# Performance work log

Measured on AMD Instinct MI355X. Metric: run time of the kernel, lower is better.

The kernel has to match this reference:

```python
import jax, jax.numpy as jnp
import numpy as np

N_NODES = 100000
N_DIH = 1000000
SCALAR_DIM = 128
HIDDEN = 64
ATTR_DIM = 3


def setup_inputs() -> dict:
    key = jax.random.key(0)
    ks = jax.random.split(key, 10)
    x = jax.random.normal(ks[0], (N_NODES, SCALAR_DIM), dtype=jnp.float32)
    quadra_index = jax.random.randint(ks[1], (4, N_DIH), 0, N_NODES, dtype=jnp.int32)
    quadra_attr = jax.random.normal(ks[2], (N_DIH, ATTR_DIM), dtype=jnp.float32)
    d_in = SCALAR_DIM * 2 + ATTR_DIM
    W1 = jax.random.normal(ks[3], (d_in, HIDDEN), dtype=jnp.float32) / np.sqrt(d_in)
    b1 = jnp.zeros((HIDDEN,), dtype=jnp.float32)
    W2 = jax.random.normal(ks[4], (HIDDEN, HIDDEN), dtype=jnp.float32) / np.sqrt(HIDDEN)
    b2 = jnp.zeros((HIDDEN,), dtype=jnp.float32)
    W3 = jax.random.normal(ks[5], (HIDDEN, SCALAR_DIM), dtype=jnp.float32) / np.sqrt(HIDDEN)
    b3 = jnp.zeros((SCALAR_DIM,), dtype=jnp.float32)
    # o3.Linear on pure scalars ('128x0e'->'128x0e') is a bias-free linear map
    Wout = jax.random.normal(ks[6], (SCALAR_DIM, SCALAR_DIM), dtype=jnp.float32) / np.sqrt(SCALAR_DIM)
    return {"x": x, "quadra_index": quadra_index, "quadra_attr": quadra_attr,
            "W1": W1, "b1": b1, "W2": W2, "b2": b2, "W3": W3, "b3": b3, "Wout": Wout}


def _scatter_mean(msgs, idx, num_segments):
    sums = jax.ops.segment_sum(msgs, idx, num_segments=num_segments)
    counts = jax.ops.segment_sum(jnp.ones((msgs.shape[0],), msgs.dtype), idx,
                                 num_segments=num_segments)
    return sums / jnp.maximum(counts, 1.0)[:, None]


def reference(x, quadra_index, quadra_attr, W1, b1, W2, b2, W3, b3, Wout):
    n = x.shape[0]
    x_scalar = x[:, :SCALAR_DIM]
    i, j, k, l = quadra_index[0], quadra_index[1], quadra_index[2], quadra_index[3]
    # gather endpoints, concat with dihedral attrs: [E, 2*D + 3]
    dih_in = jnp.concatenate([x_scalar[i], x_scalar[l], quadra_attr], axis=-1)
    h = jax.nn.silu(dih_in @ W1 + b1)
    h = jax.nn.silu(h @ W2 + b2)
    msgs = h @ W3 + b3  # [E, D]
    aggr_j = _scatter_mean(msgs, j, n)
    aggr_k = _scatter_mean(msgs, k, n)
    aggr = (aggr_j + aggr_k) * 0.5
    return aggr @ Wout
```

## Files before the change

kernel.cpp:

```cpp
#include <hip/hip_runtime.h>

#define N_NODES    100000
#define N_DIH      1000000
#define SCALAR_DIM 128
#define HIDDEN     64
#define ATTR_DIM   3

typedef short v8s __attribute__((ext_vector_type(8)));
typedef float v4f __attribute__((ext_vector_type(4)));
typedef _Float16 v8h __attribute__((ext_vector_type(8)));

__device__ __forceinline__ float silu(float v) {
    return __fdividef(v, 1.0f + __expf(-v));
}

__device__ __forceinline__ unsigned short bf16_rne(float f) {
    unsigned int u = __float_as_uint(f);
    u = (u + 0x7FFFu + ((u >> 16) & 1u)) >> 16;
    return (unsigned short)u;
}

__device__ __forceinline__ float2 bf2_to_f2(unsigned int v) {
    float2 r;
    r.x = __uint_as_float(v << 16);
    r.y = __uint_as_float(v & 0xffff0000u);
    return r;
}

#define PREP_W   112
#define PREP_W34 33
#define PREP_G   64
#define PREP_H   3907
#define PREP_XB  12500
#define PREP_MAIN (PREP_W + PREP_W34 + PREP_G + PREP_H)
#define PREP_ALL  (PREP_MAIN + PREP_XB)

__global__ void prep_kernel(const float* __restrict__ x, unsigned short* __restrict__ xb,
                            const float* __restrict__ W1, const float* __restrict__ W2,
                            const float* __restrict__ W3, const float* __restrict__ b1,
                            const float* __restrict__ b3,
                            const float* __restrict__ Wout,
                            unsigned short* __restrict__ W1f, unsigned short* __restrict__ W2f,
                            unsigned short* __restrict__ W3f, unsigned short* __restrict__ W1g,
                            float* __restrict__ W34, float* __restrict__ b34,
                            float* __restrict__ PK,
                            const int* __restrict__ qidx,
                            int* __restrict__ cnt_j, int* __restrict__ cnt_k,
                            int* __restrict__ rank_j, int* __restrict__ rank_k) {
    const int b = blockIdx.x;
    if (b < PREP_W) {
        const int tid = b * 256 + threadIdx.x;
        if (tid < 16384) {
            const int j = tid & 7, lane = (tid >> 3) & 63, t = tid >> 9;
            const int k = (t >> 2) * 32 + ((lane >> 4) << 3) + j;
            const int n = (t & 3) * 16 + (lane & 15);
            W1f[tid] = bf16_rne(W1[k * 64 + n]);
        } else if (tid < 20480) {
            const int i = tid - 16384;
            const int j = i & 7, lane = (i >> 3) & 63, t = i >> 9;
            const int k = (t >> 2) * 32 + ((lane >> 4) << 3) + j;
            const int n = (t & 3) * 16 + (lane & 15);
            W2f[i] = bf16_rne(W2[k * 64 + n]);
        } else if (tid < 28672) {
            const int i = tid - 20480;
            const int j = i & 7, lane = (i >> 3) & 63, t = i >> 9;
            const int k = (t >> 3) * 32 + ((lane >> 4) << 3) + j;
            const int n = (t & 7) * 16 + (lane & 15);
            W3f[i] = bf16_rne(W3[k * 128 + n]);
        }
    } else if (b < PREP_W + PREP_W34) {
        const int t34 = (b - PREP_W) * 256 + threadIdx.x;
        if (t34 < 8192) {
            const int r = t34 >> 7, c = t34 & 127;
            float s = 0.f;
            #pragma unroll 4
            for (int m = 0; m < 128; ++m) s += W3[r * 128 + m] * Wout[m * 128 + c];
            W34[t34] = s;
        } else if (t34 < 8320) {
            const int c = t34 - 8192;
            float s = 0.f;
            #pragma unroll 4
            for (int m = 0; m < 128; ++m) s += b3[m] * Wout[m * 128 + c];
            b34[c] = s;
        } else if (t34 < 8384) {
            const int c = t34 - 8320;
            PK[c * 4 + 0] = W1[256 * 64 + c];
            PK[c * 4 + 1] = W1[257 * 64 + c];
            PK[c * 4 + 2] = W1[258 * 64 + c];
            PK[c * 4 + 3] = b1[c];
        }
    } else if (b < PREP_W + PREP_W34 + PREP_G) {
        const int i = (b - PREP_W - PREP_W34) * 256 + threadIdx.x;
        const int j = i & 7, lane = (i >> 3) & 63, t = i >> 9;
        const int k = (t >> 3) * 32 + ((lane >> 4) << 3) + j;
        const int n = (t & 7) * 16 + (lane & 15);
        const float w = (n < 64) ? W1[k * 64 + n] : W1[(128 + k) * 64 + (n - 64)];
        W1g[i] = bf16_rne(w);
    } else if (b < PREP_MAIN) {
        const int t = (b - PREP_W - PREP_W34 - PREP_G) * 256 + threadIdx.x;
        if (t < N_DIH) {
            const int rj = atomicAdd(&cnt_j[qidx[N_DIH + t]], 1);
            const int rk = atomicAdd(&cnt_k[qidx[2 * N_DIH + t]], 1);
            if (rank_j != nullptr) {
                rank_j[t] = rj;
                rank_k[t] = rk;
            }
        }
    } else {
        const int t = (b - PREP_MAIN) * 256 + threadIdx.x;
        const float4 v = *(const float4*)&x[(size_t)t * 4];
        ushort4 o;
        o.x = bf16_rne(v.x); o.y = bf16_rne(v.y); o.z = bf16_rne(v.z); o.w = bf16_rne(v.w);
        *(ushort4*)&xb[(size_t)t * 4] = o;
    }
}

__global__ __launch_bounds__(1024) void scan_kernel(const int* __restrict__ cnt_j,
                                                    const int* __restrict__ cnt_k,
                                                    int* __restrict__ off_j, int* __restrict__ off_k) {
    const int* cnt = blockIdx.x ? cnt_k : cnt_j;
    int* off = blockIdx.x ? off_k : off_j;
    __shared__ int wtot[17];
    const int tid = threadIdx.x, lane = tid & 63, wv = tid >> 6;
    int carry = 0;
    for (int base = 0; base < N_NODES; base += 1024) {
        const int i = base + tid;
        const int v = (i < N_NODES) ? cnt[i] : 0;
        int inc = v;
        #pragma unroll
        for (int o = 1; o < 64; o <<= 1) {
            const int t = __shfl_up(inc, o);
            if (lane >= o) inc += t;
        }
        if (lane == 63) wtot[wv] = inc;
        __syncthreads();
        if (tid == 0) {
            int run = 0;
            #pragma unroll
            for (int w = 0; w < 16; ++w) { const int t = wtot[w]; wtot[w] = run; run += t; }
            wtot[16] = run;
        }
        __syncthreads();
        const int excl = inc - v + wtot[wv] + carry;
        if (i < N_NODES) off[i] = excl;
        carry += wtot[16];
        __syncthreads();
    }
    if (tid == 0) off[N_NODES] = carry;
}

__global__ void permute_kernel(const int* __restrict__ qidx,
                               const int* __restrict__ off_j, const int* __restrict__ off_k,
                               const int* __restrict__ rank_j, const int* __restrict__ rank_k,
                               int* __restrict__ perm_j, int* __restrict__ perm_k) {
    const int t = blockIdx.x * blockDim.x + threadIdx.x;
    if (t < N_DIH) {
        const int j = qidx[N_DIH + t];
        perm_j[off_j[j] + rank_j[t]] = t;
        const int k = qidx[2 * N_DIH + t];
        perm_k[off_k[k] + rank_k[t]] = t;
    }
}

#define UVW 3125

__global__ __launch_bounds__(256, 4) void uv_kernel(
    const float* __restrict__ x, const unsigned short* __restrict__ W1g,
    _Float16* __restrict__ uv)
{
    const int tid = threadIdx.x, lane = tid & 63, wv = tid >> 6;
    const int g = blockIdx.x * 4 + wv;
    if (g >= UVW) return;
    const int D0 = g * 32;
    const int m16 = lane & 15, quad = lane >> 4;
    const int r0 = D0 + m16, r1 = D0 + 16 + m16;

    v4f acc[2][8];
    #pragma unroll
    for (int mt = 0; mt < 2; ++mt)
        #pragma unroll
        for (int nt = 0; nt < 8; ++nt) acc[mt][nt] = (v4f){0.f, 0.f, 0.f, 0.f};

    #pragma unroll
    for (int kc = 0; kc < 4; ++kc) {
        const int co = kc * 32 + quad * 8;
        v8s a0, a1;
        {
            const float4 f0 = *(const float4*)&x[(size_t)r0 * 128 + co];
            const float4 f1 = *(const float4*)&x[(size_t)r0 * 128 + co + 4];
            a0[0] = (short)bf16_rne(f0.x); a0[1] = (short)bf16_rne(f0.y);
            a0[2] = (short)bf16_rne(f0.z); a0[3] = (short)bf16_rne(f0.w);
            a0[4] = (short)bf16_rne(f1.x); a0[5] = (short)bf16_rne(f1.y);
            a0[6] = (short)bf16_rne(f1.z); a0[7] = (short)bf16_rne(f1.w);
        }
        {
            const float4 f0 = *(const float4*)&x[(size_t)r1 * 128 + co];
            const float4 f1 = *(const float4*)&x[(size_t)r1 * 128 + co + 4];
            a1[0] = (short)bf16_rne(f0.x); a1[1] = (short)bf16_rne(f0.y);
            a1[2] = (short)bf16_rne(f0.z); a1[3] = (short)bf16_rne(f0.w);
            a1[4] = (short)bf16_rne(f1.x); a1[5] = (short)bf16_rne(f1.y);
            a1[6] = (short)bf16_rne(f1.z); a1[7] = (short)bf16_rne(f1.w);
        }
        #pragma unroll
        for (int nt = 0; nt < 8; ++nt) {
            const v8s bf = *(const v8s*)(W1g + ((kc * 8 + nt) * 64 + lane) * 8);
            acc[0][nt] = __builtin_amdgcn_mfma_f32_16x16x32_bf16(a0, bf, acc[0][nt], 0, 0, 0);
            acc[1][nt] = __builtin_amdgcn_mfma_f32_16x16x32_bf16(a1, bf, acc[1][nt], 0, 0, 0);
        }
    }
    #pragma unroll
    for (int mt = 0; mt < 2; ++mt)
        #pragma unroll
        for (int nt = 0; nt < 8; ++nt) {
            const int c = nt * 16 + m16;
            #pragma unroll
            for (int reg = 0; reg < 4; ++reg) {
                const int n = D0 + mt * 16 + quad * 4 + reg;
                uv[(size_t)n * 128 + c] = (_Float16)acc[mt][nt][reg];
            }
        }
}

#define NW16 62500

__global__ __launch_bounds__(256, 6) void mlp2s_kernel(
    const _Float16* __restrict__ uv, const int* __restrict__ qidx,
    const float* __restrict__ attr, const float* __restrict__ PK,
    const unsigned short* __restrict__ W2f, const float* __restrict__ b2,
    const int* __restrict__ off_j, const int* __restrict__ off_k,
    const int* __restrict__ rank_j, const int* __restrict__ rank_k,
    unsigned short* __restrict__ h2j, unsigned short* __restrict__ h2k)
{
    __shared__ __align__(16) unsigned short hbuf[4][1024];
    const int tid = threadIdx.x, lane = tid & 63, wv = tid >> 6;
    const int g = blockIdx.x * 4 + wv;
    const int D0 = g * 16;
    const int m16 = lane & 15, quad = lane >> 4;
    unsigned short* hs = hbuf[wv];

    const int d = D0 + m16;
    const int irow = qidx[d];
    const int lrow = qidx[3 * N_DIH + d];
    const int jn = qidx[N_DIH + d];
    const int kn = qidx[2 * N_DIH + d];
    const int pj = off_j[jn] + rank_j[d];
    const int pk = off_k[kn] + rank_k[d];

    const _Float16* up = uv + (size_t)irow * 128 + quad * 8;
    const _Float16* vp = uv + (size_t)lrow * 128 + 64 + quad * 8;
    const v8h u0 = *(const v8h*)(up + 0);
    const v8h u1 = *(const v8h*)(up + 32);
    const v8h w0 = *(const v8h*)(vp + 0);
    const v8h w1 = *(const v8h*)(vp + 32);
    const float a0 = attr[(size_t)d * 3 + 0];
    const float a1 = attr[(size_t)d * 3 + 1];
    const float a2 = attr[(size_t)d * 3 + 2];

    const int cb = quad * 8;
    v8s af0, af1;
    #pragma unroll
    for (int e = 0; e < 8; ++e) {
        const float4 pk0 = *(const float4*)&PK[(size_t)(cb + e) * 4];
        const float s0 = (float)u0[e] + (float)w0[e] + pk0.x * a0 + pk0.y * a1 + pk0.z * a2 + pk0.w;
        af0[e] = (short)bf16_rne(silu(s0));
        const float4 pk1 = *(const float4*)&PK[(size_t)(32 + cb + e) * 4];
        const float s1 = (float)u1[e] + (float)w1[e] + pk1.x * a0 + pk1.y * a1 + pk1.z * a2 + pk1.w;
        af1[e] = (short)bf16_rne(silu(s1));
    }

    v4f acc2[4];
    #pragma unroll
    for (int nt = 0; nt < 4; ++nt) acc2[nt] = (v4f){0.f, 0.f, 0.f, 0.f};
    #pragma unroll
    for (int nt = 0; nt < 4; ++nt) {
        const v8s bA = *(const v8s*)(W2f + ((nt) * 64 + lane) * 8);
        const v8s bB = *(const v8s*)(W2f + ((4 + nt) * 64 + lane) * 8);
        acc2[nt] = __builtin_amdgcn_mfma_f32_16x16x32_bf16(af0, bA, acc2[nt], 0, 0, 0);
        acc2[nt] = __builtin_amdgcn_mfma_f32_16x16x32_bf16(af1, bB, acc2[nt], 0, 0, 0);
    }

    #pragma unroll
    for (int nt = 0; nt < 4; ++nt) {
        const int c = nt * 16 + m16;
        const float b2c = b2[c];
        #pragma unroll
        for (int reg = 0; reg < 4; ++reg) {
            const int row = quad * 4 + reg;
            hs[row * 64 + c] = bf16_rne(silu(acc2[nt][reg] + b2c));
        }
    }
    const int sub = lane & 7;
    #pragma unroll
    for (int i = 0; i < 2; ++i) {
        const int row = i * 8 + (lane >> 3);
        const int pjr = __shfl(pj, row);
        const int pkr = __shfl(pk, row);
        const v8s rowv = *(const v8s*)(hs + i * 512 + lane * 8);
        *(v8s*)(h2j + (size_t)pjr * 64 + sub * 8) = rowv;
        *(v8s*)(h2k + (size_t)pkr * 64 + sub * 8) = rowv;
    }
}

__global__ __launch_bounds__(256, 8) void mlp2_kernel(
    const _Float16* __restrict__ uv, const int* __restrict__ qidx,
    const float* __restrict__ attr, const float* __restrict__ PK,
    const unsigned short* __restrict__ W2f, const float* __restrict__ b2,
    unsigned short* __restrict__ h2)
{
    __shared__ __align__(16) unsigned short hbuf[4][1024];
    const int tid = threadIdx.x, lane = tid & 63, wv = tid >> 6;
    const int g = blockIdx.x * 4 + wv;
    const int D0 = g * 16;
    const int m16 = lane & 15, quad = lane >> 4;
    unsigned short* hs = hbuf[wv];

    const int d = D0 + m16;
    const int irow = qidx[d];
    const int lrow = qidx[3 * N_DIH + d];

    const _Float16* up = uv + (size_t)irow * 128 + quad * 8;
    const _Float16* vp = uv + (size_t)lrow * 128 + 64 + quad * 8;
    const v8h u0 = *(const v8h*)(up + 0);
    const v8h u1 = *(const v8h*)(up + 32);
    const v8h w0 = *(const v8h*)(vp + 0);
    const v8h w1 = *(const v8h*)(vp + 32);
    const float a0 = attr[(size_t)d * 3 + 0];
    const float a1 = attr[(size_t)d * 3 + 1];
    const float a2 = attr[(size_t)d * 3 + 2];

    const int cb = quad * 8;
    v8s af0, af1;
    #pragma unroll
    for (int e = 0; e < 8; ++e) {
        const float4 pk0 = *(const float4*)&PK[(size_t)(cb + e) * 4];
        const float s0 = (float)u0[e] + (float)w0[e] + pk0.x * a0 + pk0.y * a1 + pk0.z * a2 + pk0.w;
        af0[e] = (short)bf16_rne(silu(s0));
        const float4 pk1 = *(const float4*)&PK[(size_t)(32 + cb + e) * 4];
        const float s1 = (float)u1[e] + (float)w1[e] + pk1.x * a0 + pk1.y * a1 + pk1.z * a2 + pk1.w;
        af1[e] = (short)bf16_rne(silu(s1));
    }

    v4f acc2[4];
    #pragma unroll
    for (int nt = 0; nt < 4; ++nt) acc2[nt] = (v4f){0.f, 0.f, 0.f, 0.f};
    #pragma unroll
    for (int nt = 0; nt < 4; ++nt) {
        const v8s bA = *(const v8s*)(W2f + ((nt) * 64 + lane) * 8);
        const v8s bB = *(const v8s*)(W2f + ((4 + nt) * 64 + lane) * 8);
        acc2[nt] = __builtin_amdgcn_mfma_f32_16x16x32_bf16(af0, bA, acc2[nt], 0, 0, 0);
        acc2[nt] = __builtin_amdgcn_mfma_f32_16x16x32_bf16(af1, bB, acc2[nt], 0, 0, 0);
    }

    #pragma unroll
    for (int nt = 0; nt < 4; ++nt) {
        const int c = nt * 16 + m16;
        const float b2c = b2[c];
        #pragma unroll
        for (int reg = 0; reg < 4; ++reg) {
            const int row = quad * 4 + reg;
            hs[row * 64 + c] = bf16_rne(silu(acc2[nt][reg] + b2c));
        }
    }
    #pragma unroll
    for (int i = 0; i < 2; ++i) {
        const v8s row16 = *(const v8s*)(hs + i * 512 + lane * 8);
        *(v8s*)(h2 + (size_t)D0 * 64 + i * 512 + lane * 8) = row16;
    }
}

#define NWAVES 31250

__global__ __launch_bounds__(256, 8) void mlp12_kernel(
    const unsigned short* __restrict__ xb, const int* __restrict__ qidx,
    const float* __restrict__ attr,
    const float* __restrict__ W1, const float* __restrict__ b1,
    const float* __restrict__ b2,
    const unsigned short* __restrict__ W1f, const unsigned short* __restrict__ W2f,
    unsigned short* __restrict__ h2)
{
    __shared__ __align__(16) unsigned short hbuf[4][1024];
    const int tid  = threadIdx.x;
    const int lane = tid & 63;
    const int wv   = tid >> 6;
    const int g    = blockIdx.x * 4 + wv;
    const int D0   = g * 16;
    const int m16  = lane & 15;
    const int quad = lane >> 4;
    unsigned short* hs = hbuf[wv];

    const int irow = qidx[D0 + m16];
    const int lrow = qidx[3 * N_DIH + D0 + m16];

    v4f acc[4];
    #pragma unroll
    for (int nt = 0; nt < 4; ++nt) acc[nt] = (v4f){0.f, 0.f, 0.f, 0.f};

    #pragma unroll
    for (int kc = 0; kc < 8; ++kc) {
        const int side = kc >> 2;
        const int coff = (kc & 3) * 32 + quad * 8;
        const int r0 = side ? lrow : irow;
        const v8s a0 = *(const v8s*)(xb + (size_t)r0 * 128 + coff);
        #pragma unroll
        for (int nt = 0; nt < 4; ++nt) {
            const v8s b = *(const v8s*)(W1f + ((kc * 4 + nt) * 64 + lane) * 8);
            acc[nt] = __builtin_amdgcn_mfma_f32_16x16x32_bf16(a0, b, acc[nt], 0, 0, 0);
        }
    }

    #pragma unroll
    for (int nt = 0; nt < 4; ++nt) {
        const int c = nt * 16 + m16;
        const float b1c = b1[c];
        const float wa0 = W1[256 * 64 + c];
        const float wa1 = W1[257 * 64 + c];
        const float wa2 = W1[258 * 64 + c];
        const int quadp = (nt * 2 + (m16 >> 3)) & 3;
        const int jp    = m16 & 7;
        const int kc2   = nt >> 1;
        #pragma unroll
        for (int reg = 0; reg < 4; ++reg) {
            const int r = quad * 4 + reg;
            const int d = D0 + r;
            float v = acc[nt][reg] + b1c
                    + attr[(size_t)d * 3 + 0] * wa0
                    + attr[(size_t)d * 3 + 1] * wa1
                    + attr[(size_t)d * 3 + 2] * wa2;
            v = silu(v);
            hs[kc2 * 512 + (r + 16 * quadp) * 8 + jp] = bf16_rne(v);
        }
    }

    v4f acc2[4];
    #pragma unroll
    for (int nt = 0; nt < 4; ++nt) acc2[nt] = (v4f){0.f, 0.f, 0.f, 0.f};

    #pragma unroll
    for (int kc = 0; kc < 2; ++kc) {
        const v8s a0 = *(const v8s*)(hs + kc * 512 + lane * 8);
        #pragma unroll
        for (int nt = 0; nt < 4; ++nt) {
            const v8s b = *(const v8s*)(W2f + ((kc * 4 + nt) * 64 + lane) * 8);
            acc2[nt] = __builtin_amdgcn_mfma_f32_16x16x32_bf16(a0, b, acc2[nt], 0, 0, 0);
        }
    }

    #pragma unroll
    for (int nt = 0; nt < 4; ++nt) {
        const int c = nt * 16 + m16;
        const float b2c = b2[c];
        #pragma unroll
        for (int reg = 0; reg < 4; ++reg) {
            const int row = quad * 4 + reg;
            hs[row * 64 + c] = bf16_rne(silu(acc2[nt][reg] + b2c));
        }
    }
    #pragma unroll
    for (int i = 0; i < 2; ++i) {
        const v8s row16 = *(const v8s*)(hs + i * 512 + lane * 8);
        *(v8s*)(h2 + (size_t)D0 * 64 + i * 512 + lane * 8) = row16;
    }
}

__global__ __launch_bounds__(256, 2) void aggregate_seq(
    const unsigned short* __restrict__ h2j, const unsigned short* __restrict__ h2k,
    const int* __restrict__ off_j, const int* __restrict__ off_k,
    const float* __restrict__ W34, const float* __restrict__ b34,
    float* __restrict__ out)
{
    __shared__ float a_lds[64 * 132];
    const int tid    = threadIdx.x;
    const int lane   = tid & 63;
    const int wv     = __builtin_amdgcn_readfirstlane(tid >> 6);
    const int base   = blockIdx.x * 64;
    const int half   = lane >> 5;
    const int lane31 = lane & 31;

    for (int p = 0; p < 16; ++p) {
        const int ln = wv * 16 + p;
        const int n  = base + ln;
        float sx = 0.f, sy = 0.f, bf = 0.f;
        if (n < N_NODES) {
            int cj, ck;
            {
                const int e0 = off_j[n], e1 = off_j[n + 1];
                cj = e1 - e0;
                float ax = 0.f, ay = 0.f;
                int e = e0;
                for (; e + 4 <= e1; e += 4) {
                    const float2 fA = bf2_to_f2(*(const unsigned int*)(h2j + (size_t)(e + half) * 64 + lane31 * 2));
                    const float2 fB = bf2_to_f2(*(const unsigned int*)(h2j + (size_t)(e + 2 + half) * 64 + lane31 * 2));
                    ax += fA.x + fB.x; ay += fA.y + fB.y;
                }
                if (e + 2 <= e1) {
                    const float2 f = bf2_to_f2(*(const unsigned int*)(h2j + (size_t)(e + half) * 64 + lane31 * 2));
                    ax += f.x; ay += f.y;
                    e += 2;
                }
                if (e < e1 && half == 0) {
                    const float2 f = bf2_to_f2(*(const unsigned int*)(h2j + (size_t)e * 64 + lane31 * 2));
                    ax += f.x; ay += f.y;
                }
                ax += __shfl_xor(ax, 32);
                ay += __shfl_xor(ay, 32);
                const float inv = 1.0f / (float)max(cj, 1);
                sx += ax * inv; sy += ay * inv;
            }
            {
                const int e0 = off_k[n], e1 = off_k[n + 1];
                ck = e1 - e0;
                float ax = 0.f, ay = 0.f;
                int e = e0;
                for (; e + 4 <= e1; e += 4) {
                    const float2 fA = bf2_to_f2(*(const unsigned int*)(h2k + (size_t)(e + half) * 64 + lane31 * 2));
                    const float2 fB = bf2_to_f2(*(const unsigned int*)(h2k + (size_t)(e + 2 + half) * 64 + lane31 * 2));
                    ax += fA.x + fB.x; ay += fA.y + fB.y;
                }
                if (e + 2 <= e1) {
                    const float2 f = bf2_to_f2(*(const unsigned int*)(h2k + (size_t)(e + half) * 64 + lane31 * 2));
                    ax += f.x; ay += f.y;
                    e += 2;
                }
                if (e < e1 && half == 0) {
                    const float2 f = bf2_to_f2(*(const unsigned int*)(h2k + (size_t)e * 64 + lane31 * 2));
                    ax += f.x; ay += f.y;
                }
                ax += __shfl_xor(ax, 32);
                ay += __shfl_xor(ay, 32);
                const float inv = 1.0f / (float)max(ck, 1);
                sx += ax * inv; sy += ay * inv;
            }
            bf = 0.5f * ((float)(cj > 0) + (float)(ck > 0));
        }
        if (half == 0) {
            float2 w; w.x = sx * 0.5f; w.y = sy * 0.5f;
            *(float2*)&a_lds[ln * 132 + 2 * lane31] = w;
            if (lane31 == 0) a_lds[ln * 132 + 128] = bf;
        }
    }
    __syncthreads();

    const int co = wv * 32;
    const float bfv = a_lds[lane * 132 + 128];
    float acc[32];
    #pragma unroll
    for (int c = 0; c < 32; ++c) acc[c] = bfv * b34[co + c];
    const float* ap = &a_lds[lane * 132];
    #pragma unroll 2
    for (int d = 0; d < 64; d += 4) {
        const float4 av = *(const float4*)&ap[d];
        const float* w0 = &W34[(d + 0) * 128 + co];
        const float* w1 = w0 + 128;
        const float* w2 = w0 + 256;
        const float* w3 = w0 + 384;
        #pragma unroll
        for (int c = 0; c < 32; ++c)
            acc[c] += av.x * w0[c] + av.y * w1[c] + av.z * w2[c] + av.w * w3[c];
    }
    __syncthreads();
    #pragma unroll
    for (int c = 0; c < 32; c += 4)
        *(float4*)&a_lds[lane * 132 + co + c] = make_float4(acc[c], acc[c+1], acc[c+2], acc[c+3]);
    __syncthreads();
    const int q4 = lane31 << 2;
    #pragma unroll
    for (int p = 0; p < 8; ++p) {
        const int ln = wv * 16 + p * 2 + half;
        const int n  = base + ln;
        if (n < N_NODES)
            *(float4*)&out[(size_t)n * 128 + q4] = *(const float4*)&a_lds[ln * 132 + q4];
    }
}

__global__ __launch_bounds__(256, 4) void aggregate_out64(
    const unsigned short* __restrict__ h2,
    const int* __restrict__ off_j, const int* __restrict__ off_k,
    const int* __restrict__ perm_j, const int* __restrict__ perm_k,
    const float* __restrict__ W34, const float* __restrict__ b34,
    float* __restrict__ out)
{
    __shared__ float a_lds[64 * 132];
    const int tid    = threadIdx.x;
    const int lane   = tid & 63;
    const int wv     = __builtin_amdgcn_readfirstlane(tid >> 6);
    const int base   = blockIdx.x * 64;
    const int half   = lane >> 5;
    const int lane31 = lane & 31;

#define AGG_BATCH(B, permp, e, e1, ax, ay) \
    if (e + B <= e1) { \
        int dd[B]; \
        _Pragma("unroll") \
        for (int q = 0; q < B; ++q) dd[q] = permp[e + q]; \
        unsigned int rr[B]; \
        _Pragma("unroll") \
        for (int q = 0; q < B; ++q) \
            rr[q] = *(const unsigned int*)(h2 + (size_t)dd[q] * 64 + lane31 * 2); \
        _Pragma("unroll") \
        for (int q = 0; q < B; ++q) { \
            const float2 f = bf2_to_f2(rr[q]); \
            ax += f.x; ay += f.y; \
        } \
        e += B; \
    }

    for (int p = 0; p < 8; ++p) {
        const int ln = wv * 16 + p * 2 + half;
        const int n  = base + ln;
        float sx = 0.f, sy = 0.f, bf = 0.f;
        if (n < N_NODES) {
            const int ej0 = off_j[n], ej1 = off_j[n + 1];
            const int ek0 = off_k[n], ek1 = off_k[n + 1];
            const int cj = ej1 - ej0, ck = ek1 - ek0;
            float axj = 0.f, ayj = 0.f, axk = 0.f, ayk = 0.f;
            int ej = ej0, ek = ek0;
            while (ej + 8 <= ej1 && ek + 8 <= ek1) {
                int dj[8], dk[8];
                #pragma unroll
                for (int q = 0; q < 8; ++q) { dj[q] = perm_j[ej + q]; dk[q] = perm_k[ek + q]; }
                unsigned int rj[8], rk[8];
                #pragma unroll
                for (int q = 0; q < 8; ++q) {
                    rj[q] = *(const unsigned int*)(h2 + (size_t)dj[q] * 64 + lane31 * 2);
                    rk[q] = *(const unsigned int*)(h2 + (size_t)dk[q] * 64 + lane31 * 2);
                }
                #pragma unroll
                for (int q = 0; q < 8; ++q) {
                    const float2 fj = bf2_to_f2(rj[q]); axj += fj.x; ayj += fj.y;
                    const float2 fk = bf2_to_f2(rk[q]); axk += fk.x; ayk += fk.y;
                }
                ej += 8; ek += 8;
            }
            for (; ej + 8 <= ej1; ) { AGG_BATCH(8, perm_j, ej, ej1, axj, ayj) }
            AGG_BATCH(4, perm_j, ej, ej1, axj, ayj)
            AGG_BATCH(2, perm_j, ej, ej1, axj, ayj)
            AGG_BATCH(1, perm_j, ej, ej1, axj, ayj)
            for (; ek + 8 <= ek1; ) { AGG_BATCH(8, perm_k, ek, ek1, axk, ayk) }
            AGG_BATCH(4, perm_k, ek, ek1, axk, ayk)
            AGG_BATCH(2, perm_k, ek, ek1, axk, ayk)
            AGG_BATCH(1, perm_k, ek, ek1, axk, ayk)
            const float invj = 1.0f / (float)max(cj, 1);
            const float invk = 1.0f / (float)max(ck, 1);
            sx = axj * invj + axk * invk;
            sy = ayj * invj + ayk * invk;
            bf = 0.5f * ((float)(cj > 0) + (float)(ck > 0));
        }
        float2 w; w.x = sx * 0.5f; w.y = sy * 0.5f;
        *(float2*)&a_lds[ln * 132 + 2 * lane31] = w;
        if (lane31 == 0) a_lds[ln * 132 + 128] = bf;
    }
#undef AGG_BATCH
    __syncthreads();

    const int co = wv * 32;
    const float bfv = a_lds[lane * 132 + 128];
    float acc[32];
    #pragma unroll
    for (int c = 0; c < 32; ++c) acc[c] = bfv * b34[co + c];
    const float* ap = &a_lds[lane * 132];
    #pragma unroll 2
    for (int d = 0; d < 64; d += 4) {
        const float4 av = *(const float4*)&ap[d];
        const float* w0 = &W34[(d + 0) * 128 + co];
        const float* w1 = w0 + 128;
        const float* w2 = w0 + 256;
        const float* w3 = w0 + 384;
        #pragma unroll
        for (int c = 0; c < 32; ++c)
            acc[c] += av.x * w0[c] + av.y * w1[c] + av.z * w2[c] + av.w * w3[c];
    }
    __syncthreads();
    #pragma unroll
    for (int c = 0; c < 32; c += 4)
        *(float4*)&a_lds[lane * 132 + co + c] = make_float4(acc[c], acc[c+1], acc[c+2], acc[c+3]);
    __syncthreads();
    const int q4 = lane31 << 2;
    #pragma unroll
    for (int p = 0; p < 8; ++p) {
        const int ln = wv * 16 + p * 2 + half;
        const int n  = base + ln;
        if (n < N_NODES)
            *(float4*)&out[(size_t)n * 128 + q4] = *(const float4*)&a_lds[ln * 132 + q4];
    }
}

__global__ void scale_kernel(const int* __restrict__ cnt_j, const int* __restrict__ cnt_k,
                             float* __restrict__ scale_j, float* __restrict__ scale_k) {
    int n = blockIdx.x * blockDim.x + threadIdx.x;
    if (n < N_NODES) {
        scale_j[n] = 0.5f / (float)max(cnt_j[n], 1);
        scale_k[n] = 0.5f / (float)max(cnt_k[n], 1);
    }
}

__global__ __launch_bounds__(256, 3) void mlp_mfma_atomic(
    const unsigned short* __restrict__ xb, const int* __restrict__ qidx,
    const float* __restrict__ attr,
    const float* __restrict__ W1, const float* __restrict__ b1,
    const float* __restrict__ b2, const float* __restrict__ b3,
    const unsigned short* __restrict__ W1f, const unsigned short* __restrict__ W2f,
    const unsigned short* __restrict__ W3f,
    const float* __restrict__ scale_j, const float* __restrict__ scale_k,
    float* __restrict__ aggr)
{
    __shared__ __align__(16) unsigned short hbuf[4][4096];
    const int tid  = threadIdx.x;
    const int lane = tid & 63;
    const int wv   = tid >> 6;
    const int g    = blockIdx.x * 4 + wv;
    if (g >= NWAVES) return;
    const int D0   = g * 32;
    const int m16  = lane & 15;
    const int quad = lane >> 4;
    unsigned short* hs = hbuf[wv];

    int irow[2], lrow[2];
    irow[0] = qidx[D0 + m16];
    irow[1] = qidx[D0 + 16 + m16];
    lrow[0] = qidx[3 * N_DIH + D0 + m16];
    lrow[1] = qidx[3 * N_DIH + D0 + 16 + m16];

    v4f acc[2][4];
    #pragma unroll
    for (int mt = 0; mt < 2; ++mt)
        #pragma unroll
        for (int nt = 0; nt < 4; ++nt) acc[mt][nt] = (v4f){0.f, 0.f, 0.f, 0.f};
    #pragma unroll
    for (int kc = 0; kc < 8; ++kc) {
        const int side = kc >> 2;
        const int coff = (kc & 3) * 32 + quad * 8;
        const int r0 = side ? lrow[0] : irow[0];
        const int r1 = side ? lrow[1] : irow[1];
        const v8s a0 = *(const v8s*)(xb + (size_t)r0 * 128 + coff);
        const v8s a1 = *(const v8s*)(xb + (size_t)r1 * 128 + coff);
        #pragma unroll
        for (int nt = 0; nt < 4; ++nt) {
            const v8s b = *(const v8s*)(W1f + ((kc * 4 + nt) * 64 + lane) * 8);
            acc[0][nt] = __builtin_amdgcn_mfma_f32_16x16x32_bf16(a0, b, acc[0][nt], 0, 0, 0);
            acc[1][nt] = __builtin_amdgcn_mfma_f32_16x16x32_bf16(a1, b, acc[1][nt], 0, 0, 0);
        }
    }
    #pragma unroll
    for (int mt = 0; mt < 2; ++mt) {
        #pragma unroll
        for (int nt = 0; nt < 4; ++nt) {
            const int c = nt * 16 + m16;
            const float b1c = b1[c];
            const float wa0 = W1[256 * 64 + c];
            const float wa1 = W1[257 * 64 + c];
            const float wa2 = W1[258 * 64 + c];
            const int quadp = (nt * 2 + (m16 >> 3)) & 3;
            const int jp    = m16 & 7;
            const int kc2   = nt >> 1;
            #pragma unroll
            for (int reg = 0; reg < 4; ++reg) {
                const int r = quad * 4 + reg;
                const int d = D0 + mt * 16 + r;
                float v = acc[mt][nt][reg] + b1c
                        + attr[(size_t)d * 3 + 0] * wa0
                        + attr[(size_t)d * 3 + 1] * wa1
                        + attr[(size_t)d * 3 + 2] * wa2;
                v = silu(v);
                hs[mt * 1024 + kc2 * 512 + (r + 16 * quadp) * 8 + jp] = bf16_rne(v);
            }
        }
    }
    v4f acc2[2][4];
    #pragma unroll
    for (int mt = 0; mt < 2; ++mt)
        #pragma unroll
        for (int nt = 0; nt < 4; ++nt) acc2[mt][nt] = (v4f){0.f, 0.f, 0.f, 0.f};
    #pragma unroll
    for (int kc = 0; kc < 2; ++kc) {
        const v8s a0 = *(const v8s*)(hs +        kc * 512 + lane * 8);
        const v8s a1 = *(const v8s*)(hs + 1024 + kc * 512 + lane * 8);
        #pragma unroll
        for (int nt = 0; nt < 4; ++nt) {
            const v8s b = *(const v8s*)(W2f + ((kc * 4 + nt) * 64 + lane) * 8);
            acc2[0][nt] = __builtin_amdgcn_mfma_f32_16x16x32_bf16(a0, b, acc2[0][nt], 0, 0, 0);
            acc2[1][nt] = __builtin_amdgcn_mfma_f32_16x16x32_bf16(a1, b, acc2[1][nt], 0, 0, 0);
        }
    }
    #pragma unroll
    for (int mt = 0; mt < 2; ++mt) {
        #pragma unroll
        for (int nt = 0; nt < 4; ++nt) {
            const float b2c = b2[nt * 16 + m16];
            const int quadp = (nt * 2 + (m16 >> 3)) & 3;
            const int jp    = m16 & 7;
            const int kc2   = nt >> 1;
            #pragma unroll
            for (int reg = 0; reg < 4; ++reg) {
                const int r = quad * 4 + reg;
                const float v = silu(acc2[mt][nt][reg] + b2c);
                hs[2048 + mt * 1024 + kc2 * 512 + (r + 16 * quadp) * 8 + jp] = bf16_rne(v);
            }
        }
    }
    v4f acc3[2][8];
    #pragma unroll
    for (int mt = 0; mt < 2; ++mt)
        #pragma unroll
        for (int nt = 0; nt < 8; ++nt) acc3[mt][nt] = (v4f){0.f, 0.f, 0.f, 0.f};
    #pragma unroll
    for (int kc = 0; kc < 2; ++kc) {
        const v8s a0 = *(const v8s*)(hs + 2048 +        kc * 512 + lane * 8);
        const v8s a1 = *(const v8s*)(hs + 2048 + 1024 + kc * 512 + lane * 8);
        #pragma unroll
        for (int nt = 0; nt < 8; ++nt) {
            const v8s b = *(const v8s*)(W3f + ((kc * 8 + nt) * 64 + lane) * 8);
            acc3[0][nt] = __builtin_amdgcn_mfma_f32_16x16x32_bf16(a0, b, acc3[0][nt], 0, 0, 0);
            acc3[1][nt] = __builtin_amdgcn_mfma_f32_16x16x32_bf16(a1, b, acc3[1][nt], 0, 0, 0);
        }
    }
    #pragma unroll
    for (int mt = 0; mt < 2; ++mt) {
        int jn[4], kn[4]; float sjv[4], skv[4];
        #pragma unroll
        for (int reg = 0; reg < 4; ++reg) {
            const int d = D0 + mt * 16 + quad * 4 + reg;
            jn[reg] = qidx[N_DIH + d];
            kn[reg] = qidx[2 * N_DIH + d];
            sjv[reg] = scale_j[jn[reg]];
            skv[reg] = scale_k[kn[reg]];
        }
        #pragma unroll
        for (int nt = 0; nt < 8; ++nt) {
            const int c = nt * 16 + m16;
            const float b3c = b3[c];
            #pragma unroll
            for (int reg = 0; reg < 4; ++reg) {
                const float v = acc3[mt][nt][reg] + b3c;
                atomicAdd(&aggr[(size_t)jn[reg] * 128 + c], v * sjv[reg]);
                atomicAdd(&aggr[(size_t)kn[reg] * 128 + c], v * skv[reg]);
            }
        }
    }
}

#define OB    256
#define OTILE 64
__global__ __launch_bounds__(OB, 2) void out_kernel(const float* __restrict__ aggr,
                                                    const float* __restrict__ Wout,
                                                    float* __restrict__ out) {
    __shared__ float a_lds[OTILE * 132];
    const int tid  = threadIdx.x;
    const int lane = tid & 63;
    const int wv   = __builtin_amdgcn_readfirstlane(tid >> 6);
    const int base = blockIdx.x * OTILE;
    const int half = lane >> 5;
    const int q4   = (lane & 31) << 2;
    #pragma unroll
    for (int p = 0; p < 8; ++p) {
        const int ln = wv * 16 + p * 2 + half;
        const int n  = base + ln;
        float4 v = make_float4(0.f, 0.f, 0.f, 0.f);
        if (n < N_NODES) v = *(const float4*)&aggr[(size_t)n * 128 + q4];
        *(float4*)&a_lds[ln * 132 + q4] = v;
    }
    __syncthreads();
    const int c0 = wv * 32;
    float acc[32];
    #pragma unroll
    for (int c = 0; c < 32; ++c) acc[c] = 0.0f;
    const float* ap = &a_lds[lane * 132];
    #pragma unroll 2
    for (int d = 0; d < 128; d += 4) {
        const float4 av = *(const float4*)&ap[d];
        const float* w0 = &Wout[(d + 0) * 128 + c0];
        const float* w1 = &Wout[(d + 1) * 128 + c0];
        const float* w2 = &Wout[(d + 2) * 128 + c0];
        const float* w3 = &Wout[(d + 3) * 128 + c0];
        #pragma unroll
        for (int c = 0; c < 32; ++c)
            acc[c] += av.x * w0[c] + av.y * w1[c] + av.z * w2[c] + av.w * w3[c];
    }
    __syncthreads();
    #pragma unroll
    for (int c = 0; c < 32; c += 4)
        *(float4*)&a_lds[lane * 132 + c0 + c] = make_float4(acc[c], acc[c+1], acc[c+2], acc[c+3]);
    __syncthreads();
    #pragma unroll
    for (int p = 0; p < 8; ++p) {
        const int ln = wv * 16 + p * 2 + half;
        const int n  = base + ln;
        if (n < N_NODES)
            *(float4*)&out[(size_t)n * 128 + q4] = *(const float4*)&a_lds[ln * 132 + q4];
    }
}

extern "C" void kernel_launch(void* const* d_in, const int* in_sizes, int n_in,
                              void* d_out, int out_size, void* d_ws, size_t ws_size,
                              hipStream_t stream) {
    const float* x    = (const float*)d_in[0];
    const int*   qidx = (const int*)d_in[1];
    const float* attr = (const float*)d_in[2];
    const float* W1   = (const float*)d_in[3];
    const float* b1   = (const float*)d_in[4];
    const float* W2   = (const float*)d_in[5];
    const float* b2   = (const float*)d_in[6];
    const float* W3   = (const float*)d_in[7];
    const float* b3   = (const float*)d_in[8];
    const float* Wout = (const float*)d_in[9];
    float* out = (float*)d_out;
    float* wsf = (float*)d_ws;

    const size_t words = ws_size / 4;
    if (words >= (size_t)79300000) {
        size_t o = 0;
        unsigned short* h2j = (unsigned short*)wsf;          o += 32000000;
        unsigned short* h2k = (unsigned short*)(wsf + o);    o += 32000000;
        _Float16* uvp = (_Float16*)(wsf + o);                o += 12800000;
        unsigned short* W1f = (unsigned short*)(wsf + o);    o += 8192;
        unsigned short* W2f = (unsigned short*)(wsf + o);    o += 2048;
        unsigned short* W3f = (unsigned short*)(wsf + o);    o += 4096;
        unsigned short* W1g = (unsigned short*)(wsf + o);    o += 8192;
        float* W34  = wsf + o;                               o += 8192;
        float* b34  = wsf + o;                               o += 128;
        float* PK   = wsf + o;                               o += 256;
        int* cnt_j  = (int*)(wsf + o);                       o += 100000;
        int* cnt_k  = (int*)(wsf + o);                       o += 100000;
        int* off_j  = (int*)(wsf + o);                       o += 100001;
        int* off_k  = (int*)(wsf + o);                       o += 100001;
        int* rank_j = (int*)(wsf + o);                       o += 1000000;
        int* rank_k = (int*)(wsf + o);                       o += 1000000;

        hipMemsetAsync(cnt_j, 0, (size_t)200000 * sizeof(int), stream);
        prep_kernel<<<PREP_MAIN, 256, 0, stream>>>(
            x, h2j , W1, W2, W3, b1, b3, Wout,
            W1f, W2f, W3f, W1g, W34, b34, PK, qidx, cnt_j, cnt_k, rank_j, rank_k);
        scan_kernel<<<2, 1024, 0, stream>>>(cnt_j, cnt_k, off_j, off_k);
        uv_kernel<<<(UVW + 3) / 4, 256, 0, stream>>>(x, W1g, uvp);
        mlp2s_kernel<<<NW16 / 4, 256, 0, stream>>>(
            uvp, qidx, attr, PK, W2f, b2, off_j, off_k, rank_j, rank_k, h2j, h2k);
        aggregate_seq<<<(N_NODES + 63) / 64, 256, 0, stream>>>(
            h2j, h2k, off_j, off_k, W34, b34, out);
    } else if (words >= (size_t)47500000) {
        size_t o = 0;
        unsigned short* h2  = (unsigned short*)wsf;          o += 32000000;
        _Float16* uvp = (_Float16*)(wsf + o);                o += 12800000;
        unsigned short* W1f = (unsigned short*)(wsf + o);    o += 8192;
        unsigned short* W2f = (unsigned short*)(wsf + o);    o += 2048;
        unsigned short* W3f = (unsigned short*)(wsf + o);    o += 4096;
        unsigned short* W1g = (unsigned short*)(wsf + o);    o += 8192;
        float* W34  = wsf + o;                               o += 8192;
        float* b34  = wsf + o;                               o += 128;
        float* PK   = wsf + o;                               o += 256;
        int* cnt_j  = (int*)(wsf + o);                       o += 100000;
        int* cnt_k  = (int*)(wsf + o);                       o += 100000;
        int* off_j  = (int*)(wsf + o);                       o += 100001;
        int* off_k  = (int*)(wsf + o);                       o += 100001;
        int* perm_j = (int*)(wsf + o);                       o += 1000000;
        int* perm_k = (int*)(wsf + o);                       o += 1000000;
        int* rank_j = (int*)h2;
        int* rank_k = rank_j + N_DIH;

        hipMemsetAsync(cnt_j, 0, (size_t)200000 * sizeof(int), stream);
        prep_kernel<<<PREP_MAIN, 256, 0, stream>>>(
            x, h2 , W1, W2, W3, b1, b3, Wout,
            W1f, W2f, W3f, W1g, W34, b34, PK, qidx, cnt_j, cnt_k, rank_j, rank_k);
        scan_kernel<<<2, 1024, 0, stream>>>(cnt_j, cnt_k, off_j, off_k);
        permute_kernel<<<(N_DIH + 255) / 256, 256, 0, stream>>>(
            qidx, off_j, off_k, rank_j, rank_k, perm_j, perm_k);
        uv_kernel<<<(UVW + 3) / 4, 256, 0, stream>>>(x, W1g, uvp);
        mlp2_kernel<<<NW16 / 4, 256, 0, stream>>>(uvp, qidx, attr, PK, W2f, b2, h2);
        aggregate_out64<<<(N_NODES + 63) / 64, 256, 0, stream>>>(
            h2, off_j, off_k, perm_j, perm_k, W34, b34, out);
    } else if (words >= (size_t)41100000) {
        size_t o = 0;
        unsigned short* h2  = (unsigned short*)wsf;          o += 32000000;
        unsigned short* xb  = (unsigned short*)(wsf + o);    o += 6400000;
        unsigned short* W1f = (unsigned short*)(wsf + o);    o += 8192;
        unsigned short* W2f = (unsigned short*)(wsf + o);    o += 2048;
        unsigned short* W3f = (unsigned short*)(wsf + o);    o += 4096;
        float* W34  = wsf + o;                               o += 8192;
        float* b34  = wsf + o;                               o += 128;
        int* cnt_j  = (int*)(wsf + o);                       o += 100000;
        int* cnt_k  = (int*)(wsf + o);                       o += 100000;
        int* off_j  = (int*)(wsf + o);                       o += 100001;
        int* off_k  = (int*)(wsf + o);                       o += 100001;
        int* perm_j = (int*)(wsf + o);                       o += 1000000;
        int* perm_k = (int*)(wsf + o);                       o += 1000000;
        unsigned short* W1g = (unsigned short*)(wsf + o);    o += 8192;
        float* PK   = wsf + o;                               o += 256;
        int* rank_j = (int*)h2;
        int* rank_k = rank_j + N_DIH;

        hipMemsetAsync(cnt_j, 0, (size_t)200000 * sizeof(int), stream);
        prep_kernel<<<PREP_ALL, 256, 0, stream>>>(
            x, xb, W1, W2, W3, b1, b3, Wout,
            W1f, W2f, W3f, W1g, W34, b34, PK, qidx, cnt_j, cnt_k, rank_j, rank_k);
        scan_kernel<<<2, 1024, 0, stream>>>(cnt_j, cnt_k, off_j, off_k);
        permute_kernel<<<(N_DIH + 255) / 256, 256, 0, stream>>>(
            qidx, off_j, off_k, rank_j, rank_k, perm_j, perm_k);
        mlp12_kernel<<<NW16 / 4, 256, 0, stream>>>(
            xb, qidx, attr, W1, b1, b2, W1f, W2f, h2);
        aggregate_out64<<<(N_NODES + 63) / 64, 256, 0, stream>>>(
            h2, off_j, off_k, perm_j, perm_k, W34, b34, out);
    } else {
        int*   cnt_j   = (int*)wsf;
        int*   cnt_k   = cnt_j + N_NODES;
        float* scale_j = wsf + 200000;
        float* scale_k = wsf + 300000;
        float* aggr    = wsf + 400000;
        unsigned short* xb  = (unsigned short*)(wsf + 13200000);
        unsigned short* W1f = (unsigned short*)(wsf + 19600000);
        unsigned short* W2f = (unsigned short*)(wsf + 19608192);
        unsigned short* W3f = (unsigned short*)(wsf + 19610240);
        float* W34 = wsf + 19612288;
        float* b34 = wsf + 19612288;
        unsigned short* W1g = (unsigned short*)(wsf + 19612288);
        float* PK  = wsf + 19612288;

        hipMemsetAsync(cnt_j, 0, (size_t)2 * N_NODES * sizeof(int), stream);
        hipMemsetAsync(aggr, 0, (size_t)N_NODES * 128 * sizeof(float), stream);
        prep_kernel<<<PREP_ALL, 256, 0, stream>>>(
            x, xb, W1, W2, W3, b1, b3, Wout,
            W1f, W2f, W3f, W1g, W34, b34, PK, qidx, cnt_j, cnt_k, nullptr, nullptr);
        scale_kernel<<<(N_NODES + 255) / 256, 256, 0, stream>>>(cnt_j, cnt_k, scale_j, scale_k);
        mlp_mfma_atomic<<<(NWAVES + 3) / 4, 256, 0, stream>>>(
            xb, qidx, attr, W1, b1, b2, b3, W1f, W2f, W3f, scale_j, scale_k, aggr);
        out_kernel<<<(N_NODES + OTILE - 1) / OTILE, OB, 0, stream>>>(aggr, Wout, out);
    }
}
```

Baseline: 536.3 us.

## Write hidden rows once in j-order and gather k-side through a permutation

```diff
diff --git a/kernel.cpp b/kernel.cpp
--- a/kernel.cpp
+++ b/kernel.cpp
@@ -162,6 +162,18 @@
     }
 }
 
+__global__ void permute2_kernel(const int* __restrict__ qidx,
+                                const int* __restrict__ off_j, const int* __restrict__ off_k,
+                                const int* __restrict__ rank_j, const int* __restrict__ rank_k,
+                                int* __restrict__ permk2) {
+    const int t = blockIdx.x * blockDim.x + threadIdx.x;
+    if (t < N_DIH) {
+        const int j = qidx[N_DIH + t];
+        const int k = qidx[2 * N_DIH + t];
+        permk2[off_k[k] + rank_k[t]] = off_j[j] + rank_j[t];
+    }
+}
+
 #define UVW 3125
 
 __global__ __launch_bounds__(256, 4) void uv_kernel(
@@ -223,13 +235,12 @@
 
 #define NW16 62500
 
-__global__ __launch_bounds__(256, 6) void mlp2s_kernel(
+__global__ __launch_bounds__(256, 8) void mlp2j_kernel(
     const _Float16* __restrict__ uv, const int* __restrict__ qidx,
     const float* __restrict__ attr, const float* __restrict__ PK,
     const unsigned short* __restrict__ W2f, const float* __restrict__ b2,
-    const int* __restrict__ off_j, const int* __restrict__ off_k,
-    const int* __restrict__ rank_j, const int* __restrict__ rank_k,
-    unsigned short* __restrict__ h2j, unsigned short* __restrict__ h2k)
+    const int* __restrict__ off_j, const int* __restrict__ rank_j,
+    unsigned short* __restrict__ h2j)
 {
     __shared__ __align__(16) unsigned short hbuf[4][1024];
     const int tid = threadIdx.x, lane = tid & 63, wv = tid >> 6;
@@ -242,9 +253,7 @@
     const int irow = qidx[d];
     const int lrow = qidx[3 * N_DIH + d];
     const int jn = qidx[N_DIH + d];
-    const int kn = qidx[2 * N_DIH + d];
     const int pj = off_j[jn] + rank_j[d];
-    const int pk = off_k[kn] + rank_k[d];
 
     const _Float16* up = uv + (size_t)irow * 128 + quad * 8;
     const _Float16* vp = uv + (size_t)lrow * 128 + 64 + quad * 8;
@@ -294,77 +303,8 @@
     for (int i = 0; i < 2; ++i) {
         const int row = i * 8 + (lane >> 3);
         const int pjr = __shfl(pj, row);
-        const int pkr = __shfl(pk, row);
         const v8s rowv = *(const v8s*)(hs + i * 512 + lane * 8);
         *(v8s*)(h2j + (size_t)pjr * 64 + sub * 8) = rowv;
-        *(v8s*)(h2k + (size_t)pkr * 64 + sub * 8) = rowv;
-    }
-}
-
-__global__ __launch_bounds__(256, 8) void mlp2_kernel(
-    const _Float16* __restrict__ uv, const int* __restrict__ qidx,
-    const float* __restrict__ attr, const float* __restrict__ PK,
-    const unsigned short* __restrict__ W2f, const float* __restrict__ b2,
-    unsigned short* __restrict__ h2)
-{
-    __shared__ __align__(16) unsigned short hbuf[4][1024];
-    const int tid = threadIdx.x, lane = tid & 63, wv = tid >> 6;
-    const int g = blockIdx.x * 4 + wv;
-    const int D0 = g * 16;
-    const int m16 = lane & 15, quad = lane >> 4;
-    unsigned short* hs = hbuf[wv];
-
-    const int d = D0 + m16;
-    const int irow = qidx[d];
-    const int lrow = qidx[3 * N_DIH + d];
-
-    const _Float16* up = uv + (size_t)irow * 128 + quad * 8;
-    const _Float16* vp = uv + (size_t)lrow * 128 + 64 + quad * 8;
-    const v8h u0 = *(const v8h*)(up + 0);
-    const v8h u1 = *(const v8h*)(up + 32);
-    const v8h w0 = *(const v8h*)(vp + 0);
-    const v8h w1 = *(const v8h*)(vp + 32);
-    const float a0 = attr[(size_t)d * 3 + 0];
-    const float a1 = attr[(size_t)d * 3 + 1];
-    const float a2 = attr[(size_t)d * 3 + 2];
-
-    const int cb = quad * 8;
-    v8s af0, af1;
-    #pragma unroll
-    for (int e = 0; e < 8; ++e) {
-        const float4 pk0 = *(const float4*)&PK[(size_t)(cb + e) * 4];
-        const float s0 = (float)u0[e] + (float)w0[e] + pk0.x * a0 + pk0.y * a1 + pk0.z * a2 + pk0.w;
-        af0[e] = (short)bf16_rne(silu(s0));
-        const float4 pk1 = *(const float4*)&PK[(size_t)(32 + cb + e) * 4];
-        const float s1 = (float)u1[e] + (float)w1[e] + pk1.x * a0 + pk1.y * a1 + pk1.z * a2 + pk1.w;
-        af1[e] = (short)bf16_rne(silu(s1));
-    }
-
-    v4f acc2[4];
-    #pragma unroll
-    for (int nt = 0; nt < 4; ++nt) acc2[nt] = (v4f){0.f, 0.f, 0.f, 0.f};
-    #pragma unroll
-    for (int nt = 0; nt < 4; ++nt) {
-        const v8s bA = *(const v8s*)(W2f + ((nt) * 64 + lane) * 8);
-        const v8s bB = *(const v8s*)(W2f + ((4 + nt) * 64 + lane) * 8);
-        acc2[nt] = __builtin_amdgcn_mfma_f32_16x16x32_bf16(af0, bA, acc2[nt], 0, 0, 0);
-        acc2[nt] = __builtin_amdgcn_mfma_f32_16x16x32_bf16(af1, bB, acc2[nt], 0, 0, 0);
-    }
-
-    #pragma unroll
-    for (int nt = 0; nt < 4; ++nt) {
-        const int c = nt * 16 + m16;
-        const float b2c = b2[c];
-        #pragma unroll
-        for (int reg = 0; reg < 4; ++reg) {
-            const int row = quad * 4 + reg;
-            hs[row * 64 + c] = bf16_rne(silu(acc2[nt][reg] + b2c));
-        }
-    }
-    #pragma unroll
-    for (int i = 0; i < 2; ++i) {
-        const v8s row16 = *(const v8s*)(hs + i * 512 + lane * 8);
-        *(v8s*)(h2 + (size_t)D0 * 64 + i * 512 + lane * 8) = row16;
     }
 }
 
@@ -462,9 +402,10 @@
     }
 }
 
-__global__ __launch_bounds__(256, 2) void aggregate_seq(
-    const unsigned short* __restrict__ h2j, const unsigned short* __restrict__ h2k,
+__global__ __launch_bounds__(256, 4) void aggregate_hyb(
+    const unsigned short* __restrict__ h2j,
     const int* __restrict__ off_j, const int* __restrict__ off_k,
+    const int* __restrict__ permk2,
     const float* __restrict__ W34, const float* __restrict__ b34,
     float* __restrict__ out)
 {
@@ -476,68 +417,84 @@
     const int half   = lane >> 5;
     const int lane31 = lane & 31;
 
-    for (int p = 0; p < 16; ++p) {
-        const int ln = wv * 16 + p;
+#define JS_BATCH(B) \
+    if (ej + B <= ej1) { \
+        unsigned int rr[B]; \
+        _Pragma("unroll") \
+        for (int q = 0; q < B; ++q) \
+            rr[q] = *(const unsigned int*)(h2j + (size_t)(ej + q) * 64 + lane31 * 2); \
+        _Pragma("unroll") \
+        for (int q = 0; q < B; ++q) { \
+            const float2 f = bf2_to_f2(rr[q]); \
+            axj += f.x; ayj += f.y; \
+        } \
+        ej += B; \
+    }
+
+#define KG_BATCH(B) \
+    if (ek + B <= ek1) { \
+        int dd[B]; \
+        _Pragma("unroll") \
+        for (int q = 0; q < B; ++q) dd[q] = permk2[ek + q]; \
+        unsigned int rr[B]; \
+        _Pragma("unroll") \
+        for (int q = 0; q < B; ++q) \
+            rr[q] = *(const unsigned int*)(h2j + (size_t)dd[q] * 64 + lane31 * 2); \
+        _Pragma("unroll") \
+        for (int q = 0; q < B; ++q) { \
+            const float2 f = bf2_to_f2(rr[q]); \
+            axk += f.x; ayk += f.y; \
+        } \
+        ek += B; \
+    }
+
+    for (int p = 0; p < 8; ++p) {
+        const int ln = wv * 16 + p * 2 + half;
         const int n  = base + ln;
         float sx = 0.f, sy = 0.f, bf = 0.f;
         if (n < N_NODES) {
-            int cj, ck;
-            {
-                const int e0 = off_j[n], e1 = off_j[n + 1];
-                cj = e1 - e0;
-                float ax = 0.f, ay = 0.f;
-                int e = e0;
-                for (; e + 4 <= e1; e += 4) {
-                    const float2 fA = bf2_to_f2(*(const unsigned int*)(h2j + (size_t)(e + half) * 64 + lane31 * 2));
-                    const float2 fB = bf2_to_f2(*(const unsigned int*)(h2j + (size_t)(e + 2 + half) * 64 + lane31 * 2));
-                    ax += fA.x + fB.x; ay += fA.y + fB.y;
+            const int ej0 = off_j[n], ej1 = off_j[n + 1];
+            const int ek0 = off_k[n], ek1 = off_k[n + 1];
+            const int cj = ej1 - ej0, ck = ek1 - ek0;
+            float axj = 0.f, ayj = 0.f, axk = 0.f, ayk = 0.f;
+            int ej = ej0, ek = ek0;
+            while (ej + 8 <= ej1 && ek + 8 <= ek1) {
+                int dk[8];
+                #pragma unroll
+                for (int q = 0; q < 8; ++q) dk[q] = permk2[ek + q];
+                unsigned int rj[8], rk[8];
+                #pragma unroll
+                for (int q = 0; q < 8; ++q) {
+                    rj[q] = *(const unsigned int*)(h2j + (size_t)(ej + q) * 64 + lane31 * 2);
+                    rk[q] = *(const unsigned int*)(h2j + (size_t)dk[q] * 64 + lane31 * 2);
                 }
-                if (e + 2 <= e1) {
-                    const float2 f = bf2_to_f2(*(const unsigned int*)(h2j + (size_t)(e + half) * 64 + lane31 * 2));
-                    ax += f.x; ay += f.y;
-                    e += 2;
+                #pragma unroll
+                for (int q = 0; q < 8; ++q) {
+                    const float2 fj = bf2_to_f2(rj[q]); axj += fj.x; ayj += fj.y;
+                    const float2 fk = bf2_to_f2(rk[q]); axk += fk.x; ayk += fk.y;
                 }
-                if (e < e1 && half == 0) {
-                    const float2 f = bf2_to_f2(*(const unsigned int*)(h2j + (size_t)e * 64 + lane31 * 2));
-                    ax += f.x; ay += f.y;
-                }
-                ax += __shfl_xor(ax, 32);
-                ay += __shfl_xor(ay, 32);
-                const float inv = 1.0f / (float)max(cj, 1);
-                sx += ax * inv; sy += ay * inv;
+                ej += 8; ek += 8;
             }
-            {
-                const int e0 = off_k[n], e1 = off_k[n + 1];
-                ck = e1 - e0;
-                float ax = 0.f, ay = 0.f;
-                int e = e0;
-                for (; e + 4 <= e1; e += 4) {
-                    const float2 fA = bf2_to_f2(*(const unsigned int*)(h2k + (size_t)(e + half) * 64 + lane31 * 2));
-                    const float2 fB = bf2_to_f2(*(const unsigned int*)(h2k + (size_t)(e + 2 + half) * 64 + lane31 * 2));
-                    ax += fA.x + fB.x; ay += fA.y + fB.y;
-                }
-                if (e + 2 <= e1) {
-                    const float2 f = bf2_to_f2(*(const unsigned int*)(h2k + (size_t)(e + half) * 64 + lane31 * 2));
-                    ax += f.x; ay += f.y;
-                    e += 2;
-                }
-                if (e < e1 && half == 0) {
-                    const float2 f = bf2_to_f2(*(const unsigned int*)(h2k + (size_t)e * 64 + lane31 * 2));
-                    ax += f.x; ay += f.y;
-                }
-                ax += __shfl_xor(ax, 32);
-                ay += __shfl_xor(ay, 32);
-                const float inv = 1.0f / (float)max(ck, 1);
-                sx += ax * inv; sy += ay * inv;
-            }
+            for (; ej + 8 <= ej1; ) { JS_BATCH(8) }
+            JS_BATCH(4)
+            JS_BATCH(2)
+            JS_BATCH(1)
+            for (; ek + 8 <= ek1; ) { KG_BATCH(8) }
+            KG_BATCH(4)
+            KG_BATCH(2)
+            KG_BATCH(1)
+            const float invj = 1.0f / (float)max(cj, 1);
+            const float invk = 1.0f / (float)max(ck, 1);
+            sx = axj * invj + axk * invk;
+            sy = ayj * invj + ayk * invk;
             bf = 0.5f * ((float)(cj > 0) + (float)(ck > 0));
         }
-        if (half == 0) {
-            float2 w; w.x = sx * 0.5f; w.y = sy * 0.5f;
-            *(float2*)&a_lds[ln * 132 + 2 * lane31] = w;
-            if (lane31 == 0) a_lds[ln * 132 + 128] = bf;
-        }
-    }
+        float2 w; w.x = sx * 0.5f; w.y = sy * 0.5f;
+        *(float2*)&a_lds[ln * 132 + 2 * lane31] = w;
+        if (lane31 == 0) a_lds[ln * 132 + 128] = bf;
+    }
+#undef JS_BATCH
+#undef KG_BATCH
     __syncthreads();
 
     const int co = wv * 32;
@@ -906,11 +863,10 @@
     float* wsf = (float*)d_ws;
 
     const size_t words = ws_size / 4;
-    if (words >= (size_t)79300000) {
+    if (words >= (size_t)47500000) {
         size_t o = 0;
         unsigned short* h2j = (unsigned short*)wsf;          o += 32000000;
-        unsigned short* h2k = (unsigned short*)(wsf + o);    o += 32000000;
-        _Float16* uvp = (_Float16*)(wsf + o);                o += 12800000;
+        _Float16* uvp = (_Float16*)(wsf + o);                o += 6400000;
         unsigned short* W1f = (unsigned short*)(wsf + o);    o += 8192;
         unsigned short* W2f = (unsigned short*)(wsf + o);    o += 2048;
         unsigned short* W3f = (unsigned short*)(wsf + o);    o += 4096;
@@ -924,48 +880,20 @@
         int* off_k  = (int*)(wsf + o);                       o += 100001;
         int* rank_j = (int*)(wsf + o);                       o += 1000000;
         int* rank_k = (int*)(wsf + o);                       o += 1000000;
+        int* permk2 = (int*)(wsf + o);                       o += 1000000;
 
         hipMemsetAsync(cnt_j, 0, (size_t)200000 * sizeof(int), stream);
         prep_kernel<<<PREP_MAIN, 256, 0, stream>>>(
             x, h2j , W1, W2, W3, b1, b3, Wout,
             W1f, W2f, W3f, W1g, W34, b34, PK, qidx, cnt_j, cnt_k, rank_j, rank_k);
         scan_kernel<<<2, 1024, 0, stream>>>(cnt_j, cnt_k, off_j, off_k);
+        permute2_kernel<<<(N_DIH + 255) / 256, 256, 0, stream>>>(
+            qidx, off_j, off_k, rank_j, rank_k, permk2);
         uv_kernel<<<(UVW + 3) / 4, 256, 0, stream>>>(x, W1g, uvp);
-        mlp2s_kernel<<<NW16 / 4, 256, 0, stream>>>(
-            uvp, qidx, attr, PK, W2f, b2, off_j, off_k, rank_j, rank_k, h2j, h2k);
-        aggregate_seq<<<(N_NODES + 63) / 64, 256, 0, stream>>>(
-            h2j, h2k, off_j, off_k, W34, b34, out);
-    } else if (words >= (size_t)47500000) {
-        size_t o = 0;
-        unsigned short* h2  = (unsigned short*)wsf;          o += 32000000;
-        _Float16* uvp = (_Float16*)(wsf + o);                o += 12800000;
-        unsigned short* W1f = (unsigned short*)(wsf + o);    o += 8192;
-        unsigned short* W2f = (unsigned short*)(wsf + o);    o += 2048;
-        unsigned short* W3f = (unsigned short*)(wsf + o);    o += 4096;
-        unsigned short* W1g = (unsigned short*)(wsf + o);    o += 8192;
-        float* W34  = wsf + o;                               o += 8192;
-        float* b34  = wsf + o;                               o += 128;
-        float* PK   = wsf + o;                               o += 256;
-        int* cnt_j  = (int*)(wsf + o);                       o += 100000;
-        int* cnt_k  = (int*)(wsf + o);                       o += 100000;
-        int* off_j  = (int*)(wsf + o);                       o += 100001;
-        int* off_k  = (int*)(wsf + o);                       o += 100001;
-        int* perm_j = (int*)(wsf + o);                       o += 1000000;
-        int* perm_k = (int*)(wsf + o);                       o += 1000000;
-        int* rank_j = (int*)h2;
-        int* rank_k = rank_j + N_DIH;
-
-        hipMemsetAsync(cnt_j, 0, (size_t)200000 * sizeof(int), stream);
-        prep_kernel<<<PREP_MAIN, 256, 0, stream>>>(
-            x, h2 , W1, W2, W3, b1, b3, Wout,
-            W1f, W2f, W3f, W1g, W34, b34, PK, qidx, cnt_j, cnt_k, rank_j, rank_k);
-        scan_kernel<<<2, 1024, 0, stream>>>(cnt_j, cnt_k, off_j, off_k);
-        permute_kernel<<<(N_DIH + 255) / 256, 256, 0, stream>>>(
-            qidx, off_j, off_k, rank_j, rank_k, perm_j, perm_k);
-        uv_kernel<<<(UVW + 3) / 4, 256, 0, stream>>>(x, W1g, uvp);
-        mlp2_kernel<<<NW16 / 4, 256, 0, stream>>>(uvp, qidx, attr, PK, W2f, b2, h2);
-        aggregate_out64<<<(N_NODES + 63) / 64, 256, 0, stream>>>(
-            h2, off_j, off_k, perm_j, perm_k, W34, b34, out);
+        mlp2j_kernel<<<NW16 / 4, 256, 0, stream>>>(
+            uvp, qidx, attr, PK, W2f, b2, off_j, rank_j, h2j);
+        aggregate_hyb<<<(N_NODES + 63) / 64, 256, 0, stream>>>(
+            h2j, off_j, off_k, permk2, W34, b34, out);
     } else if (words >= (size_t)41100000) {
         size_t o = 0;
         unsigned short* h2  = (unsigned short*)wsf;          o += 32000000;
```

Result: faster. 516.7 us (-3.7%).
